# Kernel optimization log

Hardware: AMD Instinct MI355X
Metric: run time of the kernel (lower is better)

Reference implementation:

```python
import jax, jax.numpy as jnp
import numpy as np

EPS = 1e-7

def _dubbed_squash(v):
    norm = jnp.linalg.norm(v, axis=-1, keepdims=True)
    coef = 1.0 - 1.0 / (jnp.exp(norm) + EPS)
    return coef * v / (norm + EPS)

def setup_inputs() -> dict:
    key = jax.random.key(0)
    k1, k2, k3 = jax.random.split(key, 3)
    B, N, dp = 16, 1152, 8   # batch, num_primary_caps, dim_primary_caps
    D, dd = 10, 16           # num_digit_caps, dim_digit_caps
    primary_caps = jax.random.normal(k1, (B, N, dp), dtype=jnp.float32)
    W = jax.random.normal(k2, (D, N, dd, dp), dtype=jnp.float32) * 0.05
    B_prior = jax.random.normal(k3, (D, 1, N), dtype=jnp.float32) * 0.05
    return {"primary_caps": primary_caps, "W": W, "B_prior": B_prior}

def reference(primary_caps, W, B_prior):
    dp = primary_caps.shape[-1]
    # votes: U_hat[b,d,n,j] = W[d,n,j,i] @ u[b,n,i]   (replaces the tf.map_fn)
    U_hat = jnp.einsum('dnji,bni->bdnj', W, primary_caps)  # [B,D,N,dd]
    # self-similarity score matrix (as in original: full NxN matmul)
    A = jnp.einsum('bdnj,bdmj->bdnm', U_hat, U_hat) / jnp.sqrt(
        jnp.asarray(dp, dtype=primary_caps.dtype))          # [B,D,N,N]
    A_sum = jnp.sum(A, axis=2, keepdims=True)               # [B,D,1,N]
    C = jax.nn.softmax(A_sum, axis=1)                       # softmax over digit axis
    # weighted combine with learned log-priors: (B+C) @ U_hat -> [B,D,1,dd] -> squeeze
    S = jnp.einsum('bdkn,bdnj->bdj', B_prior[None] + C, U_hat)  # [B,D,dd]
    return _dubbed_squash(S)
```

## Files before the change

### kernel.cpp

```cpp
#include <hip/hip_runtime.h>
#include <hip/hip_bf16.h>

constexpr int BN = 16, NN = 1152, DP = 8, ND = 10, DD = 16;
constexpr int NCH = 2;
constexpr int NBLK = NN / NCH;
constexpr int CELLS = BN * ND * DD;
constexpr int RL = 16;
constexpr int WCH = NCH * ND;

__global__ __launch_bounds__(256) void caps_T(
    const float* __restrict__ u, const float* __restrict__ W,
    float* __restrict__ Tp)
{
    __shared__ float Wl[WCH * 128];
    __shared__ float ul[BN * NCH * DP];
    const int t = threadIdx.x;
    const int n0 = blockIdx.x * NCH;

    for (int g = t; g < WCH * 32; g += 256) {
        const int c = g >> 5, w = g & 31;
        const int nn = c / ND, d = c - nn * ND;
        reinterpret_cast<float4*>(Wl)[g] =
            *reinterpret_cast<const float4*>(
                W + ((size_t)d * NN + (n0 + nn)) * (DD * DP) + w * 4);
    }
    if (t < BN * NCH * 2) {
        const int b = t >> 2, r = t & 3, nn = r >> 1, half = r & 1;
        reinterpret_cast<float4*>(ul)[t] =
            *reinterpret_cast<const float4*>(
                u + ((size_t)b * NN + (n0 + nn)) * DP + half * 4);
    }
    __syncthreads();

    const int j = t & 15, b = t >> 4;
    float Tacc[ND];
#pragma unroll
    for (int d = 0; d < ND; ++d) Tacc[d] = 0.f;

#pragma unroll
    for (int nn = 0; nn < NCH; ++nn) {
        const float4 u0 = reinterpret_cast<const float4*>(ul)[b * 4 + nn * 2];
        const float4 u1 = reinterpret_cast<const float4*>(ul)[b * 4 + nn * 2 + 1];
#pragma unroll
        for (int d = 0; d < ND; ++d) {
            const float4* wp =
                reinterpret_cast<const float4*>(Wl) + (nn * ND + d) * 32 + j * 2;
            const float4 w0 = wp[0], w1 = wp[1];
            Tacc[d] += w0.x * u0.x + w0.y * u0.y + w0.z * u0.z + w0.w * u0.w
                     + w1.x * u1.x + w1.y * u1.y + w1.z * u1.z + w1.w * u1.w;
        }
    }
    float* dst = Tp + (size_t)blockIdx.x * CELLS;
#pragma unroll
    for (int d = 0; d < ND; ++d) dst[d * 256 + t] = Tacc[d];
}

__global__ __launch_bounds__(256) void reduce_T(
    const float* __restrict__ Tp, float* __restrict__ T)
{
    __shared__ float red[256];
    const int t = threadIdx.x;
    const int cell = blockIdx.x * RL + (t & 15);
    const int cc = t >> 4;
    float s = 0.f;
    for (int k = 0; k < NBLK / RL; ++k)
        s += Tp[(size_t)(cc + RL * k) * CELLS + cell];
    red[t] = s;
    __syncthreads();
    if (t < RL) {
        float acc = 0.f;
#pragma unroll
        for (int g = 0; g < RL; ++g) acc += red[t + RL * g];
        T[blockIdx.x * RL + t] = acc;
    }
}

__global__ __launch_bounds__(256) void caps_S(
    const float* __restrict__ u, const float* __restrict__ W,
    const float* __restrict__ Bp, const float* __restrict__ T,
    float* __restrict__ Sp)
{
    __shared__ float Wl[WCH * 128];
    __shared__ float ul[BN * NCH * DP];
    __shared__ float Tl[CELLS];
    const int t = threadIdx.x;
    const int n0 = blockIdx.x * NCH;
    constexpr float RS8 = 0.35355339059327373f;

    for (int g = t; g < WCH * 32; g += 256) {
        const int c = g >> 5, w = g & 31;
        const int nn = c / ND, d = c - nn * ND;
        reinterpret_cast<float4*>(Wl)[g] =
            *reinterpret_cast<const float4*>(
                W + ((size_t)d * NN + (n0 + nn)) * (DD * DP) + w * 4);
    }
    for (int g = t; g < CELLS / 4; g += 256)
        reinterpret_cast<float4*>(Tl)[g] = reinterpret_cast<const float4*>(T)[g];
    if (t < BN * NCH * 2) {
        const int b = t >> 2, r = t & 3, nn = r >> 1, half = r & 1;
        reinterpret_cast<float4*>(ul)[t] =
            *reinterpret_cast<const float4*>(
                u + ((size_t)b * NN + (n0 + nn)) * DP + half * 4);
    }
    __syncthreads();

    const int j = t & 15, b = t >> 4;
    float Treg[ND];
#pragma unroll
    for (int q = 0; q < ND; ++q) Treg[q] = Tl[q * 256 + t];

    float Sacc[ND];
#pragma unroll
    for (int q = 0; q < ND; ++q) Sacc[q] = 0.f;

#pragma unroll
    for (int nn = 0; nn < NCH; ++nn) {
        const int n = n0 + nn;
        const float4 u0 = reinterpret_cast<const float4*>(ul)[b * 4 + nn * 2];
        const float4 u1 = reinterpret_cast<const float4*>(ul)[b * 4 + nn * 2 + 1];
        float uh[ND], a[ND];
#pragma unroll
        for (int q = 0; q < ND; ++q) {
            const float4* wp =
                reinterpret_cast<const float4*>(Wl) + (nn * ND + q) * 32 + j * 2;
            const float4 w0 = wp[0], w1 = wp[1];
            const float s =
                  w0.x * u0.x + w0.y * u0.y + w0.z * u0.z + w0.w * u0.w
                + w1.x * u1.x + w1.y * u1.y + w1.z * u1.z + w1.w * u1.w;
            uh[q] = s;
            float v = Treg[q] * s;
            v += __shfl_xor(v, 8, 16);
            v += __shfl_xor(v, 4, 16);
            v += __shfl_xor(v, 2, 16);
            v += __shfl_xor(v, 1, 16);
            a[q] = v * RS8;
        }
        float m = a[0];
#pragma unroll
        for (int q = 1; q < ND; ++q) m = fmaxf(m, a[q]);
        float e[ND], se = 0.f;
#pragma unroll
        for (int q = 0; q < ND; ++q) { e[q] = expf(a[q] - m); se += e[q]; }
        const float inv_se = 1.f / se;
#pragma unroll
        for (int q = 0; q < ND; ++q)
            Sacc[q] += (Bp[q * NN + n] + e[q] * inv_se) * uh[q];
    }
    float* dst = Sp + (size_t)blockIdx.x * CELLS;
#pragma unroll
    for (int q = 0; q < ND; ++q) dst[q * 256 + t] = Sacc[q];
}

__global__ __launch_bounds__(256) void reduce_S_out(
    const float* __restrict__ Sp, float* __restrict__ out)
{
    __shared__ float red[256];
    const int q = blockIdx.x >> 4, b = blockIdx.x & 15;
    const int t = threadIdx.x, j = t & 15, cc = t >> 4;
    const int cell = q * 256 + b * 16 + j;
    float s = 0.f;
    for (int k = 0; k < NBLK / RL; ++k)
        s += Sp[(size_t)(cc + RL * k) * CELLS + cell];
    red[t] = s;
    __syncthreads();
    if (t < RL) {
        float Sv = 0.f;
#pragma unroll
        for (int g = 0; g < RL; ++g) Sv += red[t + RL * g];
        float n2 = Sv * Sv;
#pragma unroll
        for (int off = 8; off >= 1; off >>= 1) n2 += __shfl_xor(n2, off, 16);
        const float nrm = sqrtf(n2);
        const float coef = 1.f - 1.f / (expf(nrm) + 1e-7f);
        out[((size_t)b * ND + q) * DD + t] = Sv * (coef / (nrm + 1e-7f));
    }
}

extern "C" void kernel_launch(void* const* d_in, const int* in_sizes, int n_in,
                              void* d_out, int out_size, void* d_ws, size_t ws_size,
                              hipStream_t stream) {
    const float* u  = nullptr;
    const float* W  = nullptr;
    const float* Bp = nullptr;
    for (int i = 0; i < n_in; ++i) {
        const int s = in_sizes[i];
        if (s == BN * NN * DP)            u  = (const float*)d_in[i];
        else if (s == ND * NN * DD * DP)  W  = (const float*)d_in[i];
        else if (s == ND * NN)            Bp = (const float*)d_in[i];
    }
    float* out = (float*)d_out;
    float* Tp = (float*)d_ws;
    float* T  = Tp + (size_t)NBLK * CELLS;
    float* Sp = T + CELLS;

    caps_T      <<<dim3(NBLK), 256, 0, stream>>>(u, W, Tp);
    reduce_T    <<<dim3(CELLS / RL), 256, 0, stream>>>(Tp, T);
    caps_S      <<<dim3(NBLK), 256, 0, stream>>>(u, W, Bp, T, Sp);
    reduce_S_out<<<dim3(ND * BN), 256, 0, stream>>>(Sp, out);
}
```

Measured before the change: 83.03 us.

## Fuse four kernels into one persistent kernel with software grid barriers

Merges the T-partial, T-reduce, S-partial and S-reduce/squash kernels into a single launch of 576 blocks that synchronise through atomic-counter grid barriers, with the counters zeroed by a memset. The votes are kept in registers between phases, so W is not reloaded from global memory and the votes are not recomputed in the second pass. This removes three kernel launches and the second W read. In exchange it depends on all 576 blocks being co-resident (a deadlock risk otherwise) and adds barrier spin time plus a memset.

New measurement: 324.3 us. 3.91x slower.

```diff
diff --git a/kernel.cpp b/kernel.cpp
--- a/kernel.cpp
+++ b/kernel.cpp
@@ -6,17 +6,36 @@
 constexpr int NBLK = NN / NCH;
 constexpr int CELLS = BN * ND * DD;
 constexpr int RL = 16;
+constexpr int RB = CELLS / RL;
 constexpr int WCH = NCH * ND;
 
-__global__ __launch_bounds__(256) void caps_T(
+__device__ __forceinline__ void gridbar(unsigned* __restrict__ cnt) {
+    __syncthreads();
+    if (threadIdx.x == 0) {
+        __threadfence();
+        __hip_atomic_fetch_add(cnt, 1u, __ATOMIC_ACQ_REL,
+                               __HIP_MEMORY_SCOPE_AGENT);
+        while (__hip_atomic_load(cnt, __ATOMIC_ACQUIRE,
+                                 __HIP_MEMORY_SCOPE_AGENT) < (unsigned)NBLK)
+            __builtin_amdgcn_s_sleep(1);
+        __threadfence();
+    }
+    __syncthreads();
+}
+
+__global__ __launch_bounds__(256) void caps_fused(
     const float* __restrict__ u, const float* __restrict__ W,
-    float* __restrict__ Tp)
+    const float* __restrict__ Bp, float* __restrict__ Tp,
+    float* __restrict__ T, float* __restrict__ Sp,
+    float* __restrict__ out, unsigned* __restrict__ cnt)
 {
-    __shared__ float Wl[WCH * 128];
-    __shared__ float ul[BN * NCH * DP];
-    const int t = threadIdx.x;
-    const int n0 = blockIdx.x * NCH;
+    __shared__ float sbuf[CELLS + 256];
+    const int blk = blockIdx.x, t = threadIdx.x, j = t & 15, b = t >> 4;
+    const int n0 = blk * NCH;
+    constexpr float RS8 = 0.35355339059327373f;
 
+    float* Wl = sbuf;
+    float* ul = sbuf + CELLS;
     for (int g = t; g < WCH * 32; g += 256) {
         const int c = g >> 5, w = g & 31;
         const int nn = c / ND, d = c - nn * ND;
@@ -25,18 +44,16 @@
                 W + ((size_t)d * NN + (n0 + nn)) * (DD * DP) + w * 4);
     }
     if (t < BN * NCH * 2) {
-        const int b = t >> 2, r = t & 3, nn = r >> 1, half = r & 1;
+        const int bb = t >> 2, r = t & 3, nn = r >> 1, half = r & 1;
         reinterpret_cast<float4*>(ul)[t] =
             *reinterpret_cast<const float4*>(
-                u + ((size_t)b * NN + (n0 + nn)) * DP + half * 4);
+                u + ((size_t)bb * NN + (n0 + nn)) * DP + half * 4);
     }
     __syncthreads();
 
-    const int j = t & 15, b = t >> 4;
-    float Tacc[ND];
+    float uh[NCH][ND], Tacc[ND];
 #pragma unroll
     for (int d = 0; d < ND; ++d) Tacc[d] = 0.f;
-
 #pragma unroll
     for (int nn = 0; nn < NCH; ++nn) {
         const float4 u0 = reinterpret_cast<const float4*>(ul)[b * 4 + nn * 2];
@@ -46,133 +63,107 @@
             const float4* wp =
                 reinterpret_cast<const float4*>(Wl) + (nn * ND + d) * 32 + j * 2;
             const float4 w0 = wp[0], w1 = wp[1];
-            Tacc[d] += w0.x * u0.x + w0.y * u0.y + w0.z * u0.z + w0.w * u0.w
-                     + w1.x * u1.x + w1.y * u1.y + w1.z * u1.z + w1.w * u1.w;
-        }
-    }
-    float* dst = Tp + (size_t)blockIdx.x * CELLS;
-#pragma unroll
-    for (int d = 0; d < ND; ++d) dst[d * 256 + t] = Tacc[d];
-}
-
-__global__ __launch_bounds__(256) void reduce_T(
-    const float* __restrict__ Tp, float* __restrict__ T)
-{
-    __shared__ float red[256];
-    const int t = threadIdx.x;
-    const int cell = blockIdx.x * RL + (t & 15);
-    const int cc = t >> 4;
-    float s = 0.f;
-    for (int k = 0; k < NBLK / RL; ++k)
-        s += Tp[(size_t)(cc + RL * k) * CELLS + cell];
-    red[t] = s;
-    __syncthreads();
-    if (t < RL) {
-        float acc = 0.f;
-#pragma unroll
-        for (int g = 0; g < RL; ++g) acc += red[t + RL * g];
-        T[blockIdx.x * RL + t] = acc;
-    }
-}
-
-__global__ __launch_bounds__(256) void caps_S(
-    const float* __restrict__ u, const float* __restrict__ W,
-    const float* __restrict__ Bp, const float* __restrict__ T,
-    float* __restrict__ Sp)
-{
-    __shared__ float Wl[WCH * 128];
-    __shared__ float ul[BN * NCH * DP];
-    __shared__ float Tl[CELLS];
-    const int t = threadIdx.x;
-    const int n0 = blockIdx.x * NCH;
-    constexpr float RS8 = 0.35355339059327373f;
-
-    for (int g = t; g < WCH * 32; g += 256) {
-        const int c = g >> 5, w = g & 31;
-        const int nn = c / ND, d = c - nn * ND;
-        reinterpret_cast<float4*>(Wl)[g] =
-            *reinterpret_cast<const float4*>(
-                W + ((size_t)d * NN + (n0 + nn)) * (DD * DP) + w * 4);
-    }
-    for (int g = t; g < CELLS / 4; g += 256)
-        reinterpret_cast<float4*>(Tl)[g] = reinterpret_cast<const float4*>(T)[g];
-    if (t < BN * NCH * 2) {
-        const int b = t >> 2, r = t & 3, nn = r >> 1, half = r & 1;
-        reinterpret_cast<float4*>(ul)[t] =
-            *reinterpret_cast<const float4*>(
-                u + ((size_t)b * NN + (n0 + nn)) * DP + half * 4);
-    }
-    __syncthreads();
-
-    const int j = t & 15, b = t >> 4;
-    float Treg[ND];
-#pragma unroll
-    for (int q = 0; q < ND; ++q) Treg[q] = Tl[q * 256 + t];
-
-    float Sacc[ND];
-#pragma unroll
-    for (int q = 0; q < ND; ++q) Sacc[q] = 0.f;
-
-#pragma unroll
-    for (int nn = 0; nn < NCH; ++nn) {
-        const int n = n0 + nn;
-        const float4 u0 = reinterpret_cast<const float4*>(ul)[b * 4 + nn * 2];
-        const float4 u1 = reinterpret_cast<const float4*>(ul)[b * 4 + nn * 2 + 1];
-        float uh[ND], a[ND];
-#pragma unroll
-        for (int q = 0; q < ND; ++q) {
-            const float4* wp =
-                reinterpret_cast<const float4*>(Wl) + (nn * ND + q) * 32 + j * 2;
-            const float4 w0 = wp[0], w1 = wp[1];
             const float s =
                   w0.x * u0.x + w0.y * u0.y + w0.z * u0.z + w0.w * u0.w
                 + w1.x * u1.x + w1.y * u1.y + w1.z * u1.z + w1.w * u1.w;
-            uh[q] = s;
-            float v = Treg[q] * s;
-            v += __shfl_xor(v, 8, 16);
-            v += __shfl_xor(v, 4, 16);
-            v += __shfl_xor(v, 2, 16);
-            v += __shfl_xor(v, 1, 16);
-            a[q] = v * RS8;
+            uh[nn][d] = s;
+            Tacc[d] += s;
         }
-        float m = a[0];
+    }
+    {
+        float* dst = Tp + (size_t)blk * CELLS;
 #pragma unroll
-        for (int q = 1; q < ND; ++q) m = fmaxf(m, a[q]);
-        float e[ND], se = 0.f;
+        for (int d = 0; d < ND; ++d) dst[d * 256 + t] = Tacc[d];
+    }
+    gridbar(&cnt[0]);
+
+    if (blk < RB) {
+        const int cell = blk * RL + j, cc = t >> 4;
+        float s0 = 0.f, s1 = 0.f, s2 = 0.f, s3 = 0.f;
+        for (int k = 0; k < NBLK / RL; k += 4) {
+            s0 += Tp[(size_t)(cc + RL * (k + 0)) * CELLS + cell];
+            s1 += Tp[(size_t)(cc + RL * (k + 1)) * CELLS + cell];
+            s2 += Tp[(size_t)(cc + RL * (k + 2)) * CELLS + cell];
+            s3 += Tp[(size_t)(cc + RL * (k + 3)) * CELLS + cell];
+        }
+        sbuf[t] = (s0 + s1) + (s2 + s3);
+        __syncthreads();
+        if (t < RL) {
+            float acc = 0.f;
 #pragma unroll
-        for (int q = 0; q < ND; ++q) { e[q] = expf(a[q] - m); se += e[q]; }
-        const float inv_se = 1.f / se;
+            for (int g = 0; g < RL; ++g) acc += sbuf[t + RL * g];
+            T[blk * RL + t] = acc;
+        }
+    }
+    gridbar(&cnt[1]);
+
+    for (int g = t; g < CELLS / 4; g += 256)
+        reinterpret_cast<float4*>(sbuf)[g] =
+            reinterpret_cast<const float4*>(T)[g];
+    __syncthreads();
+
+    {
+        float Treg[ND];
 #pragma unroll
-        for (int q = 0; q < ND; ++q)
-            Sacc[q] += (Bp[q * NN + n] + e[q] * inv_se) * uh[q];
+        for (int q = 0; q < ND; ++q) Treg[q] = sbuf[q * 256 + t];
+        float Sacc[ND];
+#pragma unroll
+        for (int q = 0; q < ND; ++q) Sacc[q] = 0.f;
+#pragma unroll
+        for (int nn = 0; nn < NCH; ++nn) {
+            const int n = n0 + nn;
+            float a[ND];
+#pragma unroll
+            for (int q = 0; q < ND; ++q) {
+                float v = Treg[q] * uh[nn][q];
+                v += __shfl_xor(v, 8, 16);
+                v += __shfl_xor(v, 4, 16);
+                v += __shfl_xor(v, 2, 16);
+                v += __shfl_xor(v, 1, 16);
+                a[q] = v * RS8;
+            }
+            float m = a[0];
+#pragma unroll
+            for (int q = 1; q < ND; ++q) m = fmaxf(m, a[q]);
+            float e[ND], se = 0.f;
+#pragma unroll
+            for (int q = 0; q < ND; ++q) { e[q] = expf(a[q] - m); se += e[q]; }
+            const float inv_se = 1.f / se;
+#pragma unroll
+            for (int q = 0; q < ND; ++q)
+                Sacc[q] += (Bp[q * NN + n] + e[q] * inv_se) * uh[nn][q];
+        }
+        float* dst = Sp + (size_t)blk * CELLS;
+#pragma unroll
+        for (int q = 0; q < ND; ++q) dst[q * 256 + t] = Sacc[q];
     }
-    float* dst = Sp + (size_t)blockIdx.x * CELLS;
+    gridbar(&cnt[2]);
+
+    if (blk < RB) {
+        const int q = blk >> 4, bb = blk & 15, cc = t >> 4;
+        const int cell = q * 256 + bb * 16 + j;
+        float s0 = 0.f, s1 = 0.f, s2 = 0.f, s3 = 0.f;
+        for (int k = 0; k < NBLK / RL; k += 4) {
+            s0 += Sp[(size_t)(cc + RL * (k + 0)) * CELLS + cell];
+            s1 += Sp[(size_t)(cc + RL * (k + 1)) * CELLS + cell];
+            s2 += Sp[(size_t)(cc + RL * (k + 2)) * CELLS + cell];
+            s3 += Sp[(size_t)(cc + RL * (k + 3)) * CELLS + cell];
+        }
+        __syncthreads();
+        sbuf[t] = (s0 + s1) + (s2 + s3);
+        __syncthreads();
+        if (t < RL) {
+            float Sv = 0.f;
 #pragma unroll
-    for (int q = 0; q < ND; ++q) dst[q * 256 + t] = Sacc[q];
-}
-
-__global__ __launch_bounds__(256) void reduce_S_out(
-    const float* __restrict__ Sp, float* __restrict__ out)
-{
-    __shared__ float red[256];
-    const int q = blockIdx.x >> 4, b = blockIdx.x & 15;
-    const int t = threadIdx.x, j = t & 15, cc = t >> 4;
-    const int cell = q * 256 + b * 16 + j;
-    float s = 0.f;
-    for (int k = 0; k < NBLK / RL; ++k)
-        s += Sp[(size_t)(cc + RL * k) * CELLS + cell];
-    red[t] = s;
-    __syncthreads();
-    if (t < RL) {
-        float Sv = 0.f;
+            for (int g = 0; g < RL; ++g) Sv += sbuf[t + RL * g];
+            float n2 = Sv * Sv;
 #pragma unroll
-        for (int g = 0; g < RL; ++g) Sv += red[t + RL * g];
-        float n2 = Sv * Sv;
-#pragma unroll
-        for (int off = 8; off >= 1; off >>= 1) n2 += __shfl_xor(n2, off, 16);
-        const float nrm = sqrtf(n2);
-        const float coef = 1.f - 1.f / (expf(nrm) + 1e-7f);
-        out[((size_t)b * ND + q) * DD + t] = Sv * (coef / (nrm + 1e-7f));
+            for (int off = 8; off >= 1; off >>= 1)
+                n2 += __shfl_xor(n2, off, 16);
+            const float nrm = sqrtf(n2);
+            const float coef = 1.f - 1.f / (expf(nrm) + 1e-7f);
+            out[((size_t)bb * ND + q) * DD + t] = Sv * (coef / (nrm + 1e-7f));
+        }
     }
 }
 
@@ -189,12 +180,11 @@
         else if (s == ND * NN)            Bp = (const float*)d_in[i];
     }
     float* out = (float*)d_out;
-    float* Tp = (float*)d_ws;
+    unsigned* cnt = (unsigned*)d_ws;
+    float* Tp = (float*)d_ws + 4;
     float* T  = Tp + (size_t)NBLK * CELLS;
     float* Sp = T + CELLS;
 
-    caps_T      <<<dim3(NBLK), 256, 0, stream>>>(u, W, Tp);
-    reduce_T    <<<dim3(CELLS / RL), 256, 0, stream>>>(Tp, T);
-    caps_S      <<<dim3(NBLK), 256, 0, stream>>>(u, W, Bp, T, Sp);
-    reduce_S_out<<<dim3(ND * BN), 256, 0, stream>>>(Sp, out);
+    hipMemsetAsync(d_ws, 0, 4 * sizeof(unsigned), stream);
+    caps_fused<<<dim3(NBLK), 256, 0, stream>>>(u, W, Bp, Tp, T, Sp, out, cnt);
 }
```
